# Kernel optimization log

Hardware: AMD Instinct MI355X
Metric: run time of the kernel (lower is better)

Reference implementation:

```python
import jax, jax.numpy as jnp
import numpy as np

NUM_HEADS = 8
DIM = 32
BN_EPS = 1e-5


def hard_swish(x):
    return x * jnp.clip(x + 3.0, 0.0, 6.0) / 6.0


def setup_inputs() -> dict:
    key = jax.random.key(0)
    k1, k2, k3, k4, k5 = jax.random.split(key, 5)
    B, H, W, C = 32, 28, 28, 256
    F = 4 * NUM_HEADS * DIM  # 1024
    N = H * W
    return {
        "inputs": jax.random.normal(k1, (B, H, W, C), jnp.float32),
        "w_qkv": jax.random.normal(k2, (C, F), jnp.float32) * 0.02,
        "bn_scale": jax.random.normal(k3, (F,), jnp.float32),
        "attn_bias": jax.random.normal(k4, (1, 1, N, N), jnp.float32) * 0.02,
        "w_out": jax.random.normal(k5, (2 * NUM_HEADS * DIM, C), jnp.float32) * 0.02,
    }


def reference(inputs, w_qkv, bn_scale, attn_bias, w_out):
    B, H, W, C = inputs.shape
    N = H * W
    # 1x1 conv (no bias) == per-pixel GEMM
    x = jnp.einsum('bhwc,cf->bhwf', inputs, w_qkv)  # [B,H,W,4*heads*dim]
    # BatchNorm with batch statistics (use_running_average=False), scale only
    mean = x.mean(axis=(0, 1, 2))
    var = x.var(axis=(0, 1, 2))
    x = (x - mean) * jax.lax.rsqrt(var + BN_EPS) * bn_scale
    # split into q, k, v1, v2 and move heads forward: [B,heads,N,dim]
    q, k, v1, v2 = (
        t.reshape(B, N, NUM_HEADS, DIM).transpose(0, 2, 1, 3)
        for t in jnp.split(x.reshape(B, N, -1), 4, axis=-1)
    )
    v = jnp.concatenate((v1, v2), axis=-1)  # [B,heads,N,2*dim]
    # additive learned bias attention
    scores = jnp.einsum('bhnd,bhmd->bhnm', q, k) + attn_bias  # [B,heads,N,N]
    attn = jax.nn.softmax(scores, axis=-1)
    out = hard_swish(jnp.einsum('bhnm,bhmd->bhnd', attn, v))  # [B,heads,N,2*dim]
    out = out.transpose(0, 2, 1, 3).reshape(B, H, W, -1)  # [B,H,W,heads*2*dim]
    # output 1x1 conv (no bias)
    return jnp.einsum('bhwf,fc->bhwc', out, w_out)
```

## Files before the change

### kernel.cpp

```cpp
#include <hip/hip_runtime.h>
#include <hip/hip_bf16.h>

typedef unsigned short u16;
typedef __attribute__((ext_vector_type(8))) short short8;
typedef __attribute__((ext_vector_type(4))) float f32x4;

#define NPIX 784
#define RTOT 25088

__device__ __forceinline__ float bf2f(u16 u) {
    union { unsigned int i; float f; } v; v.i = ((unsigned int)u) << 16; return v.f;
}
__device__ __forceinline__ u16 f2bf(float f) {
    unsigned int x = __float_as_uint(f);
    return (u16)((x + 0x7fffu + ((x >> 16) & 1u)) >> 16);
}

__global__ __launch_bounds__(256) void tr_f2b(const float* __restrict__ src, u16* __restrict__ dst,
                                              int R, int C) {
    int idx = blockIdx.x * 256 + threadIdx.x;
    if (idx >= R * C) return;
    int j = idx / R, i = idx - j * R;
    dst[j * R + i] = f2bf(src[i * C + j]);
}

__global__ __launch_bounds__(256) void tr_f2b_hl(const float* __restrict__ src,
                                                 u16* __restrict__ dh, u16* __restrict__ dl,
                                                 int R, int C) {
    int idx = blockIdx.x * 256 + threadIdx.x;
    if (idx >= R * C) return;
    int j = idx / R, i = idx - j * R;
    float v = src[i * C + j];
    u16 h = f2bf(v);
    dh[j * R + i] = h;
    dl[j * R + i] = f2bf(v - bf2f(h));
}

__global__ __launch_bounds__(256) void gemm1_hl(const float* __restrict__ A,
                                                const u16* __restrict__ BTh, const u16* __restrict__ BTl,
                                                float* __restrict__ Cf) {
    __shared__ u16 Ah[64][32], Al[64][32], Bh[64][32], Bl[64][32];
    const int K = 256, N = 1024, Ntiles = 16;
    int bid = blockIdx.x;
    int mt = bid / Ntiles, nt = bid - mt * Ntiles;
    int m0 = mt * 64, n0 = nt * 64;
    int t = threadIdx.x;
    int lane = t & 63, w = t >> 6;
    int r = lane & 15, g = lane >> 4;
    int lrow = t >> 2, lslot = t & 3;
    f32x4 acc[4] = {};
    for (int k0 = 0; k0 < K; k0 += 32) {
        f32x4 x0 = *(const f32x4*)(A + (size_t)(m0 + lrow) * K + k0 + lslot * 8);
        f32x4 x1 = *(const f32x4*)(A + (size_t)(m0 + lrow) * K + k0 + lslot * 8 + 4);
        short8 rah, ral;
#pragma unroll
        for (int j = 0; j < 4; ++j) {
            u16 h0 = f2bf(x0[j]); rah[j] = (short)h0; ral[j] = (short)f2bf(x0[j] - bf2f(h0));
            u16 h1 = f2bf(x1[j]); rah[4 + j] = (short)h1; ral[4 + j] = (short)f2bf(x1[j] - bf2f(h1));
        }
        short8 rbh = *(const short8*)(BTh + (size_t)(n0 + lrow) * K + k0 + lslot * 8);
        short8 rbl = *(const short8*)(BTl + (size_t)(n0 + lrow) * K + k0 + lslot * 8);
        __syncthreads();
        *(short8*)&Ah[lrow][8 * (lslot ^ (lrow & 3))] = rah;
        *(short8*)&Al[lrow][8 * (lslot ^ (lrow & 3))] = ral;
        *(short8*)&Bh[lrow][8 * (lslot ^ (lrow & 3))] = rbh;
        *(short8*)&Bl[lrow][8 * (lslot ^ (lrow & 3))] = rbl;
        __syncthreads();
        short8 afh = *(const short8*)&Ah[16 * w + r][8 * (g ^ (r & 3))];
        short8 afl = *(const short8*)&Al[16 * w + r][8 * (g ^ (r & 3))];
#pragma unroll
        for (int tt = 0; tt < 4; ++tt) {
            short8 bfh = *(const short8*)&Bh[16 * tt + r][8 * (g ^ (r & 3))];
            short8 bfl = *(const short8*)&Bl[16 * tt + r][8 * (g ^ (r & 3))];
            acc[tt] = __builtin_amdgcn_mfma_f32_16x16x32_bf16(afh, bfh, acc[tt], 0, 0, 0);
            acc[tt] = __builtin_amdgcn_mfma_f32_16x16x32_bf16(afl, bfh, acc[tt], 0, 0, 0);
            acc[tt] = __builtin_amdgcn_mfma_f32_16x16x32_bf16(afh, bfl, acc[tt], 0, 0, 0);
        }
    }
#pragma unroll
    for (int tt = 0; tt < 4; ++tt)
#pragma unroll
        for (int i = 0; i < 4; ++i)
            Cf[(size_t)(m0 + 16 * w + g * 4 + i) * N + n0 + 16 * tt + r] = acc[tt][i];
}

template<int K>
__global__ __launch_bounds__(256) void gemm_bt(const u16* __restrict__ A, const u16* __restrict__ BT,
                                               float* __restrict__ Cf, int Ntiles) {
    __shared__ u16 As[64][32];
    __shared__ u16 Bs[64][32];
    int bid = blockIdx.x;
    int mt = bid / Ntiles, nt = bid - mt * Ntiles;
    int m0 = mt * 64, n0 = nt * 64;
    int t = threadIdx.x;
    int lane = t & 63, w = t >> 6;
    int r = lane & 15, g = lane >> 4;
    int lrow = t >> 2, lslot = t & 3;
    int N = Ntiles * 64;
    f32x4 acc[4] = {};
    for (int k0 = 0; k0 < K; k0 += 32) {
        short8 ra = *(const short8*)(A + (size_t)(m0 + lrow) * K + k0 + lslot * 8);
        short8 rb = *(const short8*)(BT + (size_t)(n0 + lrow) * K + k0 + lslot * 8);
        __syncthreads();
        *(short8*)&As[lrow][8 * (lslot ^ (lrow & 3))] = ra;
        *(short8*)&Bs[lrow][8 * (lslot ^ (lrow & 3))] = rb;
        __syncthreads();
        short8 af = *(const short8*)&As[16 * w + r][8 * (g ^ (r & 3))];
#pragma unroll
        for (int tt = 0; tt < 4; ++tt) {
            short8 bf = *(const short8*)&Bs[16 * tt + r][8 * (g ^ (r & 3))];
            acc[tt] = __builtin_amdgcn_mfma_f32_16x16x32_bf16(af, bf, acc[tt], 0, 0, 0);
        }
    }
#pragma unroll
    for (int tt = 0; tt < 4; ++tt)
#pragma unroll
        for (int i = 0; i < 4; ++i)
            Cf[(size_t)(m0 + 16 * w + g * 4 + i) * N + n0 + 16 * tt + r] = acc[tt][i];
}

__global__ __launch_bounds__(256) void bn_stats(const float* __restrict__ QKVf, float* __restrict__ sums) {
    int f = blockIdx.x * 256 + threadIdx.x;
    int rg = blockIdx.y;
    float s = 0.f, q = 0.f;
    for (int r = rg; r < RTOT; r += 64) {
        float x = QKVf[(size_t)r * 1024 + f];
        s += x; q += x * x;
    }
    atomicAdd(&sums[f], s);
    atomicAdd(&sums[1024 + f], q);
}

__global__ __launch_bounds__(256) void bn_scale_k(const float* __restrict__ sums, const float* __restrict__ bnsc,
                                                  float* __restrict__ scalef, float* __restrict__ meanf) {
    int f = blockIdx.x * 256 + threadIdx.x;
    float mean = sums[f] * (1.0f / RTOT);
    float var = sums[1024 + f] * (1.0f / RTOT) - mean * mean;
    scalef[f] = bnsc[f] * rsqrtf(var + 1e-5f);
    meanf[f] = mean;
}

__global__ __launch_bounds__(256) void scatter_qk(const float* __restrict__ QKVf,
                                                  const float* __restrict__ scalef, const float* __restrict__ meanf,
                                                  u16* __restrict__ Qh, u16* __restrict__ Ql,
                                                  u16* __restrict__ Kh, u16* __restrict__ Kl) {
    int idx = blockIdx.x * 256 + threadIdx.x;
    int rrow = idx >> 6;
    int c = idx & 63;
    int f0 = c * 8;
    int b = rrow / NPIX, n = rrow - b * NPIX;
    const float* x = QKVf + (size_t)rrow * 1024 + f0;
    short8 ovh, ovl;
#pragma unroll
    for (int j = 0; j < 8; ++j) {
        float y = (x[j] - meanf[f0 + j]) * scalef[f0 + j];
        u16 h = f2bf(y);
        ovh[j] = (short)h;
        ovl[j] = (short)f2bf(y - bf2f(h));
    }
    int fq = f0 & 255;
    int h = fq >> 5, d = fq & 31;
    size_t off = ((size_t)(b * 8 + h) * NPIX + n) * 32 + d;
    *(short8*)((f0 < 256 ? Qh : Kh) + off) = ovh;
    *(short8*)((f0 < 256 ? Ql : Kl) + off) = ovl;
}

__global__ __launch_bounds__(256) void scatter_v(const float* __restrict__ QKVf,
                                                 const float* __restrict__ scalef, const float* __restrict__ meanf,
                                                 u16* __restrict__ Vt) {
    __shared__ u16 T[64][16];
    int bidx = blockIdx.x;
    int bh = bidx / 49, ntile = bidx - bh * 49;
    int n0 = ntile * 16;
    int b = bh >> 3, h = bh & 7;
    int t = threadIdx.x;
    {
        int tn = t >> 4, j = t & 15, dv0 = j * 4;
        int rrow = b * NPIX + n0 + tn;
        int f = (dv0 < 32) ? (512 + h * 32 + dv0) : (768 + h * 32 + (dv0 - 32));
        f32x4 xv = *(const f32x4*)(QKVf + (size_t)rrow * 1024 + f);
#pragma unroll
        for (int jj = 0; jj < 4; ++jj)
            T[dv0 + jj][tn] = f2bf((xv[jj] - meanf[f + jj]) * scalef[f + jj]);
    }
    __syncthreads();
    {
        int dv = t >> 2, ch = (t & 3) * 4;
        u16* dst = Vt + ((size_t)bh * 64 + dv) * NPIX + n0 + ch;
#pragma unroll
        for (int jj = 0; jj < 4; ++jj)
            dst[jj] = T[dv][ch + jj];
    }
}

__global__ __launch_bounds__(256) void attn_k(const u16* __restrict__ Qh, const u16* __restrict__ Ql,
                                              const u16* __restrict__ Kh, const u16* __restrict__ Kl,
                                              const u16* __restrict__ Vt, const float* __restrict__ bias,
                                              u16* __restrict__ OUT) {
    __shared__ u16 Plds[4][16][32];
    int t = threadIdx.x;
    int w = t >> 6, lane = t & 63;
    int r = lane & 15, g = lane >> 4;
    int unit = blockIdx.x * 4 + w;
    int bh = unit / 49, qt = unit - bh * 49;
    int n0 = qt * 16;
    size_t qoff = ((size_t)bh * NPIX + n0 + r) * 32 + g * 8;
    const u16* Khb = Kh + (size_t)bh * NPIX * 32;
    const u16* Klb = Kl + (size_t)bh * NPIX * 32;
    const u16* Vbase = Vt + (size_t)bh * 64 * NPIX;

    short8 qfh = *(const short8*)(Qh + qoff);
    short8 qfl = *(const short8*)(Ql + qoff);

    f32x4 O0 = {}, O1 = {}, O2 = {}, O3 = {};
    float mrow[4], lrow[4];
#pragma unroll
    for (int i = 0; i < 4; ++i) { mrow[i] = -1e30f; lrow[i] = 0.f; }
    f32x4 zero = {};

    for (int m0 = 0; m0 < NPIX; m0 += 32) {
        bool has2 = (m0 + 16) < NPIX;
        short8 kh0 = *(const short8*)(Khb + (size_t)(m0 + r) * 32 + g * 8);
        short8 kl0 = *(const short8*)(Klb + (size_t)(m0 + r) * 32 + g * 8);
        f32x4 S0 = __builtin_amdgcn_mfma_f32_16x16x32_bf16(qfh, kh0, zero, 0, 0, 0);
        S0 = __builtin_amdgcn_mfma_f32_16x16x32_bf16(qfl, kh0, S0, 0, 0, 0);
        S0 = __builtin_amdgcn_mfma_f32_16x16x32_bf16(qfh, kl0, S0, 0, 0, 0);
        f32x4 S1 = {};
        if (has2) {
            short8 kh1 = *(const short8*)(Khb + (size_t)(m0 + 16 + r) * 32 + g * 8);
            short8 kl1 = *(const short8*)(Klb + (size_t)(m0 + 16 + r) * 32 + g * 8);
            S1 = __builtin_amdgcn_mfma_f32_16x16x32_bf16(qfh, kh1, zero, 0, 0, 0);
            S1 = __builtin_amdgcn_mfma_f32_16x16x32_bf16(qfl, kh1, S1, 0, 0, 0);
            S1 = __builtin_amdgcn_mfma_f32_16x16x32_bf16(qfh, kl1, S1, 0, 0, 0);
        }
#pragma unroll
        for (int i = 0; i < 4; ++i) {
            S0[i] += bias[(size_t)(n0 + g * 4 + i) * NPIX + m0 + r];
            if (has2) S1[i] += bias[(size_t)(n0 + g * 4 + i) * NPIX + m0 + 16 + r];
        }
        float p0[4], p1[4];
#pragma unroll
        for (int i = 0; i < 4; ++i) {
            float rm = has2 ? fmaxf(S0[i], S1[i]) : S0[i];
#pragma unroll
            for (int d = 1; d < 16; d <<= 1) rm = fmaxf(rm, __shfl_xor(rm, d, 64));
            float mn = fmaxf(mrow[i], rm);
            float ci = __expf(mrow[i] - mn);
            mrow[i] = mn;
            p0[i] = __expf(S0[i] - mn);
            p1[i] = has2 ? __expf(S1[i] - mn) : 0.f;
            float rs = p0[i] + p1[i];
#pragma unroll
            for (int d = 1; d < 16; d <<= 1) rs += __shfl_xor(rs, d, 64);
            lrow[i] = lrow[i] * ci + rs;
            O0[i] *= ci; O1[i] *= ci; O2[i] *= ci; O3[i] *= ci;
        }
#pragma unroll
        for (int i = 0; i < 4; ++i) {
            Plds[w][g * 4 + i][r] = f2bf(p0[i]);
            Plds[w][g * 4 + i][16 + r] = f2bf(p1[i]);
        }
        short8 pa = *(const short8*)&Plds[w][r][g * 8];
#pragma unroll
        for (int tt = 0; tt < 4; ++tt) {
            short8 vf = {};
            if (has2 || g < 2)
                vf = *(const short8*)(Vbase + (size_t)(16 * tt + r) * NPIX + m0 + g * 8);
            f32x4& Ot = (tt == 0 ? O0 : tt == 1 ? O1 : tt == 2 ? O2 : O3);
            Ot = __builtin_amdgcn_mfma_f32_16x16x32_bf16(pa, vf, Ot, 0, 0, 0);
        }
    }

    int b = bh >> 3, h = bh & 7;
#pragma unroll
    for (int tt = 0; tt < 4; ++tt) {
        f32x4& Ot = (tt == 0 ? O0 : tt == 1 ? O1 : tt == 2 ? O2 : O3);
#pragma unroll
        for (int i = 0; i < 4; ++i) {
            float x = Ot[i] / lrow[i];
            float hs = x * fminf(fmaxf(x + 3.f, 0.f), 6.f) * (1.f / 6.f);
            OUT[(size_t)(b * NPIX + n0 + g * 4 + i) * 512 + h * 64 + 16 * tt + r] = f2bf(hs);
        }
    }
}

extern "C" void kernel_launch(void* const* d_in, const int* in_sizes, int n_in,
                              void* d_out, int out_size, void* d_ws, size_t ws_size,
                              hipStream_t stream) {
    const float* X    = (const float*)d_in[0];
    const float* Wqkv = (const float*)d_in[1];
    const float* bnsc = (const float*)d_in[2];
    const float* bias = (const float*)d_in[3];
    const float* Wout = (const float*)d_in[4];
    float* out = (float*)d_out;
    char* ws = (char*)d_ws;

    float* QKVf   = (float*)(ws);
    u16*   OUTb   = (u16*)(ws);
    u16*   WoutT  = (u16*)(ws + 25690112);
    float* sums   = (float*)(ws + 102760448);
    float* scalef = (float*)(ws + 102768640);
    float* meanf  = (float*)(ws + 102772736);
    u16*   Qh     = (u16*)(ws + 102776832);
    u16*   Ql     = (u16*)(ws + 115621888);
    u16*   Kh     = (u16*)(ws + 128466944);
    u16*   WqkvTh = (u16*)(ws + 128466944);
    u16*   WqkvTl = (u16*)(ws + 128991232);
    u16*   Kl     = (u16*)(ws + 141312000);
    u16*   Vt     = (u16*)(ws + 154157056);

    hipMemsetAsync(sums, 0, 8192, stream);
    tr_f2b_hl<<<1024, 256, 0, stream>>>(Wqkv, WqkvTh, WqkvTl, 256, 1024);
    gemm1_hl<<<392 * 16, 256, 0, stream>>>(X, WqkvTh, WqkvTl, QKVf);
    bn_stats<<<dim3(4, 64), 256, 0, stream>>>(QKVf, sums);
    bn_scale_k<<<4, 256, 0, stream>>>(sums, bnsc, scalef, meanf);
    scatter_qk<<<6272, 256, 0, stream>>>(QKVf, scalef, meanf, Qh, Ql, Kh, Kl);
    scatter_v<<<12544, 256, 0, stream>>>(QKVf, scalef, meanf, Vt);
    tr_f2b<<<512, 256, 0, stream>>>(Wout, WoutT, 512, 256);
    attn_k<<<3136, 256, 0, stream>>>(Qh, Ql, Kh, Kl, Vt, bias, OUTb);
    gemm_bt<512><<<392 * 4, 256, 0, stream>>>(OUTb, WoutT, out, 4);
}
```

Before: 611.8 us.

## Transpose score MFMA so each lane owns a query row in online softmax

Swaps the MFMA operands so the score tile comes out transposed: each lane holds four key columns of a single query row. Row max and row sum then need only two cross-lane shuffles instead of four per row for each of four rows. The bias is read as one contiguous float4 load per lane, and the P tile is written to LDS as packed 4-element stores. This adds shuffles to broadcast the rescale factors and the final normalizers back to the output layout.

```diff
diff --git a/kernel.cpp b/kernel.cpp
--- a/kernel.cpp
+++ b/kernel.cpp
@@ -3,6 +3,7 @@
 
 typedef unsigned short u16;
 typedef __attribute__((ext_vector_type(8))) short short8;
+typedef __attribute__((ext_vector_type(4))) short s16x4;
 typedef __attribute__((ext_vector_type(4))) float f32x4;
 
 #define NPIX 784
@@ -208,58 +209,65 @@
     const u16* Khb = Kh + (size_t)bh * NPIX * 32;
     const u16* Klb = Kl + (size_t)bh * NPIX * 32;
     const u16* Vbase = Vt + (size_t)bh * 64 * NPIX;
+    const float* brow = bias + (size_t)(n0 + r) * NPIX;
 
     short8 qfh = *(const short8*)(Qh + qoff);
     short8 qfl = *(const short8*)(Ql + qoff);
 
     f32x4 O0 = {}, O1 = {}, O2 = {}, O3 = {};
-    float mrow[4], lrow[4];
-#pragma unroll
-    for (int i = 0; i < 4; ++i) { mrow[i] = -1e30f; lrow[i] = 0.f; }
+    float mrow = -1e30f, lrow = 0.f;
     f32x4 zero = {};
 
     for (int m0 = 0; m0 < NPIX; m0 += 32) {
         bool has2 = (m0 + 16) < NPIX;
         short8 kh0 = *(const short8*)(Khb + (size_t)(m0 + r) * 32 + g * 8);
         short8 kl0 = *(const short8*)(Klb + (size_t)(m0 + r) * 32 + g * 8);
-        f32x4 S0 = __builtin_amdgcn_mfma_f32_16x16x32_bf16(qfh, kh0, zero, 0, 0, 0);
-        S0 = __builtin_amdgcn_mfma_f32_16x16x32_bf16(qfl, kh0, S0, 0, 0, 0);
-        S0 = __builtin_amdgcn_mfma_f32_16x16x32_bf16(qfh, kl0, S0, 0, 0, 0);
+        f32x4 S0 = __builtin_amdgcn_mfma_f32_16x16x32_bf16(kh0, qfh, zero, 0, 0, 0);
+        S0 = __builtin_amdgcn_mfma_f32_16x16x32_bf16(kl0, qfh, S0, 0, 0, 0);
+        S0 = __builtin_amdgcn_mfma_f32_16x16x32_bf16(kh0, qfl, S0, 0, 0, 0);
         f32x4 S1 = {};
         if (has2) {
             short8 kh1 = *(const short8*)(Khb + (size_t)(m0 + 16 + r) * 32 + g * 8);
             short8 kl1 = *(const short8*)(Klb + (size_t)(m0 + 16 + r) * 32 + g * 8);
-            S1 = __builtin_amdgcn_mfma_f32_16x16x32_bf16(qfh, kh1, zero, 0, 0, 0);
-            S1 = __builtin_amdgcn_mfma_f32_16x16x32_bf16(qfl, kh1, S1, 0, 0, 0);
-            S1 = __builtin_amdgcn_mfma_f32_16x16x32_bf16(qfh, kl1, S1, 0, 0, 0);
-        }
+            S1 = __builtin_amdgcn_mfma_f32_16x16x32_bf16(kh1, qfh, zero, 0, 0, 0);
+            S1 = __builtin_amdgcn_mfma_f32_16x16x32_bf16(kl1, qfh, S1, 0, 0, 0);
+            S1 = __builtin_amdgcn_mfma_f32_16x16x32_bf16(kh1, qfl, S1, 0, 0, 0);
+        }
+        f32x4 b0 = *(const f32x4*)(brow + m0 + g * 4);
+#pragma unroll
+        for (int i = 0; i < 4; ++i) S0[i] += b0[i];
+        if (has2) {
+            f32x4 b1 = *(const f32x4*)(brow + m0 + 16 + g * 4);
+#pragma unroll
+            for (int i = 0; i < 4; ++i) S1[i] += b1[i];
+        }
+        float tm = fmaxf(fmaxf(S0[0], S0[1]), fmaxf(S0[2], S0[3]));
+        if (has2) tm = fmaxf(tm, fmaxf(fmaxf(S1[0], S1[1]), fmaxf(S1[2], S1[3])));
+        tm = fmaxf(tm, __shfl_xor(tm, 16, 64));
+        tm = fmaxf(tm, __shfl_xor(tm, 32, 64));
+        float mn = fmaxf(mrow, tm);
+        float ci = __expf(mrow - mn);
+        mrow = mn;
+        float p0[4], p1[4];
 #pragma unroll
         for (int i = 0; i < 4; ++i) {
-            S0[i] += bias[(size_t)(n0 + g * 4 + i) * NPIX + m0 + r];
-            if (has2) S1[i] += bias[(size_t)(n0 + g * 4 + i) * NPIX + m0 + 16 + r];
-        }
-        float p0[4], p1[4];
-#pragma unroll
-        for (int i = 0; i < 4; ++i) {
-            float rm = has2 ? fmaxf(S0[i], S1[i]) : S0[i];
-#pragma unroll
-            for (int d = 1; d < 16; d <<= 1) rm = fmaxf(rm, __shfl_xor(rm, d, 64));
-            float mn = fmaxf(mrow[i], rm);
-            float ci = __expf(mrow[i] - mn);
-            mrow[i] = mn;
             p0[i] = __expf(S0[i] - mn);
             p1[i] = has2 ? __expf(S1[i] - mn) : 0.f;
-            float rs = p0[i] + p1[i];
-#pragma unroll
-            for (int d = 1; d < 16; d <<= 1) rs += __shfl_xor(rs, d, 64);
-            lrow[i] = lrow[i] * ci + rs;
-            O0[i] *= ci; O1[i] *= ci; O2[i] *= ci; O3[i] *= ci;
-        }
-#pragma unroll
-        for (int i = 0; i < 4; ++i) {
-            Plds[w][g * 4 + i][r] = f2bf(p0[i]);
-            Plds[w][g * 4 + i][16 + r] = f2bf(p1[i]);
-        }
+        }
+        float rs = (p0[0] + p0[1]) + (p0[2] + p0[3]) + ((p1[0] + p1[1]) + (p1[2] + p1[3]));
+        rs += __shfl_xor(rs, 16, 64);
+        rs += __shfl_xor(rs, 32, 64);
+        lrow = lrow * ci + rs;
+        float cre[4];
+#pragma unroll
+        for (int i = 0; i < 4; ++i) cre[i] = __shfl(ci, g * 4 + i, 64);
+#pragma unroll
+        for (int i = 0; i < 4; ++i) { O0[i] *= cre[i]; O1[i] *= cre[i]; O2[i] *= cre[i]; O3[i] *= cre[i]; }
+        s16x4 pk0, pk1;
+#pragma unroll
+        for (int i = 0; i < 4; ++i) { pk0[i] = (short)f2bf(p0[i]); pk1[i] = (short)f2bf(p1[i]); }
+        *(s16x4*)&Plds[w][r][g * 4] = pk0;
+        *(s16x4*)&Plds[w][r][16 + g * 4] = pk1;
         short8 pa = *(const short8*)&Plds[w][r][g * 8];
 #pragma unroll
         for (int tt = 0; tt < 4; ++tt) {
@@ -271,13 +279,16 @@
         }
     }
 
+    float li[4];
+#pragma unroll
+    for (int i = 0; i < 4; ++i) li[i] = 1.0f / __shfl(lrow, g * 4 + i, 64);
     int b = bh >> 3, h = bh & 7;
 #pragma unroll
     for (int tt = 0; tt < 4; ++tt) {
         f32x4& Ot = (tt == 0 ? O0 : tt == 1 ? O1 : tt == 2 ? O2 : O3);
 #pragma unroll
         for (int i = 0; i < 4; ++i) {
-            float x = Ot[i] / lrow[i];
+            float x = Ot[i] * li[i];
             float hs = x * fminf(fmaxf(x + 3.f, 0.f), 6.f) * (1.f / 6.f);
             OUT[(size_t)(b * NPIX + n0 + g * 4 + i) * 512 + h * 64 + 16 * tt + r] = f2bf(hs);
         }
@@ -309,7 +320,7 @@
     u16*   Kl     = (u16*)(ws + 141312000);
     u16*   Vt     = (u16*)(ws + 154157056);
 
-    hipMemsetAsync(sums, 0, 8192, stream);
+    (void)hipMemsetAsync(sums, 0, 8192, stream);
     tr_f2b_hl<<<1024, 256, 0, stream>>>(Wqkv, WqkvTh, WqkvTl, 256, 1024);
     gemm1_hl<<<392 * 16, 256, 0, stream>>>(X, WqkvTh, WqkvTl, QKVf);
     bn_stats<<<dim3(4, 64), 256, 0, stream>>>(QKVf, sums);
```

Result: faster. 532.8 us (-12.9%).
